# Kernel optimization log

Hardware: AMD Instinct MI355X
Metric: run time of the kernel (lower is better)

Reference implementation:

```python
import jax, jax.numpy as jnp
import numpy as np

H = 16      # query heads
KV = 8      # kv heads
D = 128     # head_dim
HID = 2048  # hidden_size
T = 2048    # tokens
EPS = 1e-6
THETA = 1000000.0


def setup_inputs() -> dict:
    key = jax.random.key(0)
    ks = jax.random.split(key, 4)
    return {
        "hidden_states": jax.random.normal(ks[0], (T, HID), jnp.float32),
        "positions": jnp.arange(T, dtype=jnp.int32),
        "qkv_w": jax.random.normal(ks[1], (H * D + 2 * KV * D, HID), jnp.float32) * 0.02,
        "o_w": jax.random.normal(ks[2], (HID, H * D), jnp.float32) * 0.02,
        "q_norm_w": jnp.ones((D,), jnp.float32),
        "k_norm_w": jnp.ones((D,), jnp.float32),
    }


def _rmsnorm(x, w):
    # x: [T, heads, D]; normalize over last dim
    var = jnp.mean(x * x, axis=-1, keepdims=True)
    return x * jax.lax.rsqrt(var + EPS) * w


def _rope(x, positions):
    # neox-style rotate-half; x: [T, heads, D]
    half = D // 2
    inv_freq = 1.0 / (THETA ** (jnp.arange(0, half, dtype=jnp.float32) / half * 1.0))
    inv_freq = 1.0 / (THETA ** (jnp.arange(0, D, 2, dtype=jnp.float32) / D))
    ang = positions.astype(jnp.float32)[:, None] * inv_freq  # [T, D/2]
    cos = jnp.cos(ang)[:, None, :]
    sin = jnp.sin(ang)[:, None, :]
    x1, x2 = x[..., :half], x[..., half:]
    return jnp.concatenate([x1 * cos - x2 * sin, x2 * cos + x1 * sin], axis=-1)


def reference(hidden_states, positions, qkv_w, o_w, q_norm_w, k_norm_w):
    scale = D ** -0.5
    qkv = hidden_states @ qkv_w.T  # [T, H*D + 2*KV*D]
    q = qkv[:, : H * D].reshape(T, H, D)
    k = qkv[:, H * D : H * D + KV * D].reshape(T, KV, D)
    v = qkv[:, H * D + KV * D :].reshape(T, KV, D)

    q = _rope(_rmsnorm(q, q_norm_w), positions)
    k = _rope(_rmsnorm(k, k_norm_w), positions)

    # GQA: repeat kv heads to match query heads
    rep = H // KV
    k = jnp.repeat(k, rep, axis=1)  # [T, H, D]
    v = jnp.repeat(v, rep, axis=1)

    scores = jnp.einsum("thd,shd->hts", q, k) * scale  # [H, T, T]
    causal = positions[:, None] >= positions[None, :]  # [T, T]
    scores = jnp.where(causal[None, :, :], scores, jnp.float32(-1e30))
    p = jax.nn.softmax(scores, axis=-1)
    o = jnp.einsum("hts,shd->thd", p, v).reshape(T, H * D)
    return o @ o_w.T  # [T, HID]
```

## Files before the change

kernel.cpp:

```cpp
#include <hip/hip_runtime.h>
#include <math.h>

#define T_TOK 2048
#define HID 2048
#define NH 16
#define NKV 8
#define HD 128
#define QKV_N 4096
#define EPS 1e-6f

typedef unsigned short u16;
typedef unsigned int   u32;
typedef __attribute__((ext_vector_type(8))) u16   u16x8;
typedef __attribute__((ext_vector_type(8))) short short8;
typedef __attribute__((ext_vector_type(4))) float floatx4;
typedef __attribute__((ext_vector_type(4))) u32   u32x4;

__device__ __forceinline__ u16 f2bf(float x) {
    u32 u = __float_as_uint(x);
    u = (u + 0x7fffu + ((u >> 16) & 1u)) >> 16;
    return (u16)u;
}
__device__ __forceinline__ float bf2f(u16 h) {
    return __uint_as_float(((u32)h) << 16);
}

__global__ __launch_bounds__(256) void cvt_f32_bf16(
    const float* __restrict__ in, u16* __restrict__ out)
{
    const size_t i = ((size_t)blockIdx.x * 256 + threadIdx.x) * 8;
    float4 a = *(const float4*)(in + i);
    float4 b = *(const float4*)(in + i + 4);
    u16x8 o;
    o[0] = f2bf(a.x); o[1] = f2bf(a.y); o[2] = f2bf(a.z); o[3] = f2bf(a.w);
    o[4] = f2bf(b.x); o[5] = f2bf(b.y); o[6] = f2bf(b.z); o[7] = f2bf(b.w);
    *(u16x8*)(out + i) = o;
}

#define GBM 256
#define GBN 128
#define GBK 64
#define BUFSH 24576

#define WAITV6 asm volatile("s_waitcnt vmcnt(6)" ::: "memory")
#define WAITV0 asm volatile("s_waitcnt vmcnt(0)" ::: "memory")
#define LGKM0  asm volatile("s_waitcnt lgkmcnt(0)" ::: "memory")
#define BARR   asm volatile("s_barrier" ::: "memory")
#define SB     __builtin_amdgcn_sched_barrier(0)

#define STAGEU(i, tt, dstb) \
    __builtin_amdgcn_global_load_lds( \
        (const __attribute__((address_space(1))) u32*)(gsrc[i] + (size_t)(tt)*GBK), \
        (__attribute__((address_space(3))) u32*)((dstb) + loff[i]), 16, 0, 0)

#define RD_A(dst, srcb, f) do { \
    dst[0] = *(const short8*)((srcb) + arow + (f)*1024 + achunk0); \
    dst[1] = *(const short8*)((srcb) + arow + (f)*1024 + achunk1); } while (0)

#define RD_B(dst, srcb) do { \
    _Pragma("unroll") \
    for (int j_ = 0; j_ < 4; ++j_) { \
        dst[j_][0] = *(const short8*)((srcb) + 16384 + brow + j_*1024 + achunk0); \
        dst[j_][1] = *(const short8*)((srcb) + 16384 + brow + j_*1024 + achunk1); } } while (0)

#define MM(f, aa, bb) do { \
    __builtin_amdgcn_s_setprio(1); \
    _Pragma("unroll") \
    for (int j_ = 0; j_ < 4; ++j_) { \
        acc[f][j_] = __builtin_amdgcn_mfma_f32_16x16x32_bf16(aa[0], bb[j_][0], acc[f][j_], 0, 0, 0); \
        acc[f][j_] = __builtin_amdgcn_mfma_f32_16x16x32_bf16(aa[1], bb[j_][1], acc[f][j_], 0, 0, 0); } \
    __builtin_amdgcn_s_setprio(0); } while (0)

#define TILE(t, CURB, NXTB, THDB, BBC, BBN) do { \
    const bool st_ = (t) + 2 < nt; \
    if (st_) { STAGEU(0, (t)+2, THDB); STAGEU(1, (t)+2, THDB); } \
    RD_A(aP1, CURB, 1); SB; \
    MM(0, aP0, BBC); SB; \
    if (st_) { STAGEU(2, (t)+2, THDB); STAGEU(3, (t)+2, THDB); } \
    RD_A(aP0, CURB, 2); SB; \
    MM(1, aP1, BBC); SB; \
    if (st_) { STAGEU(4, (t)+2, THDB); STAGEU(5, (t)+2, THDB); } \
    RD_A(aP1, CURB, 3); SB; \
    MM(2, aP0, BBC); \
    if ((t) + 1 < nt) { \
        if (st_) { WAITV6; } else { WAITV0; } \
        LGKM0; BARR; SB; \
        RD_B(BBN, NXTB); RD_A(aP0, NXTB, 0); \
    } \
    SB; \
    MM(3, aP1, BBC); SB; \
} while (0)

template<bool OUT_BF16>
__global__ __launch_bounds__(512, 2) void gemm_bt_8p(
    const u16* __restrict__ A, const u16* __restrict__ B,
    void* __restrict__ Cv, int K, int lda, int ldb, int ldc)
{
    extern __shared__ short lds[];
    const int tid = threadIdx.x;
    const int w  = tid >> 6;
    const int l  = tid & 63;
    const int m0 = blockIdx.y * GBM;
    const int n0 = blockIdx.x * GBN;
    const int mr = (w >> 1) * 64;
    const int nc = (w & 1) * 64;
    const int cc = l & 15;
    const int q4 = l >> 4;

    const int lr = l >> 3;
    const int gchunk = ((l & 7) ^ (lr & 7)) * 8;
    const u16* gsrc[6]; int loff[6];
    #pragma unroll
    for (int i = 0; i < 6; ++i) {
        const int u = w * 6 + i;
        if (u < 32) {
            gsrc[i] = A + (size_t)(m0 + u*8 + lr) * lda + gchunk;
            loff[i] = u * 512;
        } else {
            const int v = u - 32;
            gsrc[i] = B + (size_t)(n0 + v*8 + lr) * ldb + gchunk;
            loff[i] = 16384 + v * 512;
        }
    }

    const int achunk0 = ((q4)     ^ (cc & 7)) * 8;
    const int achunk1 = ((4 + q4) ^ (cc & 7)) * 8;
    const int arow = (mr + cc) * 64;
    const int brow = (nc + cc) * 64;

    floatx4 acc[4][4];
    #pragma unroll
    for (int f = 0; f < 4; ++f)
        #pragma unroll
        for (int j = 0; j < 4; ++j) acc[f][j] = (floatx4){0.f, 0.f, 0.f, 0.f};

    short8 aP0[2], aP1[2], bbE[4][2], bbO[4][2];
    short* b0 = lds;
    short* b1 = lds + BUFSH;
    short* b2 = lds + 2 * BUFSH;
    const int nt = K >> 6;

    #pragma unroll
    for (int i = 0; i < 6; ++i) STAGEU(i, 0, b0);
    #pragma unroll
    for (int i = 0; i < 6; ++i) STAGEU(i, 1, b1);
    WAITV6; BARR; SB;
    RD_B(bbE, b0); RD_A(aP0, b0, 0);

    short *CURB = b0, *NXTB = b1, *THDB = b2;
    for (int t = 0; t < nt; t += 2) {
        TILE(t, CURB, NXTB, THDB, bbE, bbO);
        { short* tmp = CURB; CURB = NXTB; NXTB = THDB; THDB = tmp; }
        TILE(t + 1, CURB, NXTB, THDB, bbO, bbE);
        { short* tmp = CURB; CURB = NXTB; NXTB = THDB; THDB = tmp; }
    }

    const int r0 = q4 * 4;
    #pragma unroll
    for (int f = 0; f < 4; ++f)
        #pragma unroll
        for (int j = 0; j < 4; ++j)
            #pragma unroll
            for (int r = 0; r < 4; ++r) {
                const int row = m0 + mr + f*16 + r0 + r;
                const int col = n0 + nc + j*16 + cc;
                if (OUT_BF16)
                    ((u16*)Cv)[(size_t)row * ldc + col] = f2bf(acc[f][j][r]);
                else
                    ((float*)Cv)[(size_t)row * ldc + col] = acc[f][j][r];
            }
}

__global__ __launch_bounds__(256) void prep(
    u16* __restrict__ qkv, const int* __restrict__ positions,
    const float* __restrict__ qw, const float* __restrict__ kw,
    u16* __restrict__ Kp, u16* __restrict__ Vtp)
{
    const int tile = blockIdx.x, kvh = blockIdx.y;
    const int tid = threadIdx.x;
    const int w = tid >> 6, l = tid & 63;
    const int t0 = tile * 64;

    const float qw0 = qw[2*l], qw1 = qw[2*l+1];
    const float kw0 = kw[2*l], kw1 = kw[2*l+1];
    const int   i0  = (2*l) & 63;
    const float if0 = exp2f(-(float)i0     * 0.311430758895690f);
    const float if1 = exp2f(-(float)(i0+1) * 0.311430758895690f);

    for (int rr = w; rr < 64; rr += 4) {
        const int t = t0 + rr;
        const int pos = positions[t];
        const float a0 = (float)pos * if0;
        const float a1 = (float)pos * if1;
        const float s0 = sinf(a0), c0 = cosf(a0);
        const float s1 = sinf(a1), c1 = cosf(a1);

        #pragma unroll
        for (int pass = 0; pass < 3; ++pass) {
            const int off = (pass < 2) ? (2*kvh + pass)*HD : NH*HD + kvh*HD;
            const float w0 = (pass < 2) ? qw0 : kw0;
            const float w1 = (pass < 2) ? qw1 : kw1;
            u16* p = qkv + (size_t)t*QKV_N + off;

            const u32 pk = *(const u32*)(p + 2*l);
            const float x0 = bf2f((u16)pk), x1 = bf2f((u16)(pk >> 16));
            float ss = x0*x0 + x1*x1;
            #pragma unroll
            for (int x = 1; x < 64; x <<= 1) ss += __shfl_xor(ss, x);
            const float rs = rsqrtf(ss * (1.0f/128.0f) + EPS);
            const float xn0 = x0 * rs * w0, xn1 = x1 * rs * w1;
            const float px0 = __shfl_xor(xn0, 32);
            const float px1 = __shfl_xor(xn1, 32);

            float o0, o1;
            if (l < 32) { o0 = xn0*c0 - px0*s0; o1 = xn1*c1 - px1*s1; }
            else        { o0 = xn0*c0 + px0*s0; o1 = xn1*c1 + px1*s1; }
            const u32 outpk = (u32)f2bf(o0) | ((u32)f2bf(o1) << 16);

            if (pass < 2) {
                *(u32*)(p + 2*l) = outpk;
            } else {
                const int ch = l >> 2;
                u16* dst = Kp + ((size_t)(kvh*32 + tile)*64 + rr)*128
                              + (ch ^ (rr & 15))*8 + (l & 3)*2;
                *(u32*)dst = outpk;
            }
        }
    }

    __shared__ u16 tl[64][136];
    {
        const int t  = tid >> 2;
        const int c0 = (tid & 3) * 32;
        const u16* src = qkv + (size_t)(t0 + t)*QKV_N + NH*HD + NKV*HD + kvh*HD + c0;
        #pragma unroll
        for (int p2 = 0; p2 < 4; ++p2)
            *(u16x8*)(&tl[t][c0 + p2*8]) = *(const u16x8*)(src + p2*8);
    }
    __syncthreads();
    {
        u16* dstb = Vtp + (size_t)(kvh*32 + tile) * 128 * 64;
        #pragma unroll
        for (int i = 0; i < 4; ++i) {
            const int id = tid*4 + i;
            const int d = id >> 3;
            const int o = id & 7;
            const int sb = (o ^ (d & 7)) * 8;
            u16x8 v;
            #pragma unroll
            for (int j = 0; j < 8; ++j) v[j] = tl[sb + j][d];
            *(u16x8*)(dstb + d*64 + o*8) = v;
        }
    }
}

__global__ __launch_bounds__(512) void attn_mfma(
    const u16* __restrict__ qkv, const u16* __restrict__ Kp,
    const u16* __restrict__ Vtp,
    u16* __restrict__ Opart, float2* __restrict__ ml)
{
    const int id   = blockIdx.x;
    const int half = id >> 8;
    const int kvh  = id & 7;
    const int bid  = (id & 255) >> 3;
    const int qt   = half ? bid : 31 - bid;
    const int t0   = qt * 64;
    const int tid  = threadIdx.x;
    const int w    = tid >> 6;
    const int l    = tid & 63;
    const int q4   = l >> 4;
    const int c    = l & 15;
    const int h    = kvh*2 + (w >> 2);
    const int wq   = w & 3;

    __shared__ short Ks[2][64 * 128];
    __shared__ short Vts[2][128 * 64];

    short8 bq[4];
    {
        const u16* qrow = qkv + (size_t)(t0 + wq*16 + c) * QKV_N + h*HD;
        #pragma unroll
        for (int kk = 0; kk < 4; ++kk)
            bq[kk] = *(const short8*)(qrow + kk*32 + q4*8);
    }

    float m_run = -3.0e38f, l_run = 0.f;
    floatx4 accO[8];
    #pragma unroll
    for (int db = 0; db < 8; ++db) accO[db] = (floatx4){0.f, 0.f, 0.f, 0.f};

    const float Cs = 0.12751744f;

    const int nt  = qt + 1;
    const int nh0 = (nt + 1) >> 1;
    const int tlo = half ? nh0 : 0;
    const int thi = half ? nt  : nh0;

    auto issue = [&](int tile, int buf) {
        const size_t tb = (size_t)(kvh*32 + tile) * 8192;
        const u16* g = (w < 4 ? Kp + tb + w*2048 : Vtp + tb + (w-4)*2048) + l*8;
        short* p = (w < 4) ? (Ks[buf] + w*2048) : (Vts[buf] + (w-4)*2048);
        #pragma unroll
        for (int i = 0; i < 4; ++i)
            __builtin_amdgcn_global_load_lds(
                (const __attribute__((address_space(1))) u32*)(g + i*512),
                (__attribute__((address_space(3))) u32*)(p + i*512), 16, 0, 0);
    };

    if (tlo < thi) issue(tlo, 0);
    int cur = 0;

    for (int tile = tlo; tile < thi; ++tile) {
        __syncthreads();
        if (tile + 1 < thi) issue(tile + 1, cur ^ 1);

        const short* Kc = Ks[cur];
        const short* Vc = Vts[cur];

        floatx4 accS[4];
        #pragma unroll
        for (int sb = 0; sb < 4; ++sb) accS[sb] = (floatx4){0.f, 0.f, 0.f, 0.f};
        #pragma unroll
        for (int kk = 0; kk < 4; ++kk) {
            #pragma unroll
            for (int sb = 0; sb < 4; ++sb) {
                short8 ak = *(const short8*)(Kc + (sb*16 + c)*128 + ((kk*4 + q4) ^ c)*8);
                accS[sb] = __builtin_amdgcn_mfma_f32_16x16x32_bf16(ak, bq[kk], accS[sb], 0, 0, 0);
            }
        }

        if (tile == qt) {
            #pragma unroll
            for (int sb = 0; sb < 4; ++sb)
                #pragma unroll
                for (int r = 0; r < 4; ++r) {
                    const int s_loc = sb*16 + q4*4 + r;
                    const int t_loc = wq*16 + c;
                    if (s_loc > t_loc) accS[sb][r] = -1.0e30f;
                }
        }

        float mt = -3.0e38f;
        #pragma unroll
        for (int sb = 0; sb < 4; ++sb)
            #pragma unroll
            for (int r = 0; r < 4; ++r) mt = fmaxf(mt, accS[sb][r]);
        mt = fmaxf(mt, __shfl_xor(mt, 16));
        mt = fmaxf(mt, __shfl_xor(mt, 32));

        const float m_new = fmaxf(m_run, mt);
        const float alpha = exp2f((m_run - m_new) * Cs);
        m_run = m_new;

        float P[4][4];
        float lsum = 0.f;
        #pragma unroll
        for (int sb = 0; sb < 4; ++sb)
            #pragma unroll
            for (int r = 0; r < 4; ++r) {
                const float e = exp2f((accS[sb][r] - m_new) * Cs);
                P[sb][r] = e;
                lsum += e;
            }
        lsum += __shfl_xor(lsum, 16);
        lsum += __shfl_xor(lsum, 32);
        l_run = l_run * alpha + lsum;

        #pragma unroll
        for (int r = 0; r < 4; ++r) {
            const float ar = __shfl(alpha, (l & 48) | (q4*4 + r));
            #pragma unroll
            for (int db = 0; db < 8; ++db) accO[db][r] *= ar;
        }

        u32 Pp[4][2];
        #pragma unroll
        for (int sb = 0; sb < 4; ++sb)
            #pragma unroll
            for (int p = 0; p < 2; ++p)
                Pp[sb][p] = (u32)f2bf(P[sb][2*p]) | ((u32)f2bf(P[sb][2*p+1]) << 16);

        const int src0 = ((2*q4    ) & 3) * 16 + c;
        const int src1 = ((2*q4 + 1) & 3) * 16 + c;
        const bool hiq = q4 >= 2;
        #pragma unroll
        for (int k2 = 0; k2 < 2; ++k2) {
            u32 x0 = __shfl(Pp[2*k2][0],   src0), y0 = __shfl(Pp[2*k2+1][0], src0);
            u32 x1 = __shfl(Pp[2*k2][1],   src0), y1 = __shfl(Pp[2*k2+1][1], src0);
            u32 x2 = __shfl(Pp[2*k2][0],   src1), y2 = __shfl(Pp[2*k2+1][0], src1);
            u32 x3 = __shfl(Pp[2*k2][1],   src1), y3 = __shfl(Pp[2*k2+1][1], src1);
            u32x4 av;
            av.x = hiq ? y0 : x0;  av.y = hiq ? y1 : x1;
            av.z = hiq ? y2 : x2;  av.w = hiq ? y3 : x3;
            const short8 aP = __builtin_bit_cast(short8, av);
            #pragma unroll
            for (int db = 0; db < 8; ++db) {
                short8 bv = *(const short8*)(Vc + (db*16 + c)*64 + (((k2*4 + q4) ^ (c & 7)))*8);
                accO[db] = __builtin_amdgcn_mfma_f32_16x16x32_bf16(aP, bv, accO[db], 0, 0, 0);
            }
        }
        cur ^= 1;
    }

    const size_t pbase = (size_t)(half * NH + h) * T_TOK;
    #pragma unroll
    for (int r = 0; r < 4; ++r) {
        const int qloc = q4*4 + r;
        const float mr = __shfl(m_run, (l & 48) | qloc);
        const float lr = __shfl(l_run, (l & 48) | qloc);
        const int row_g = t0 + wq*16 + qloc;
        u16* op = Opart + (pbase + row_g) * HD;
        #pragma unroll
        for (int db = 0; db < 8; ++db)
            op[db*16 + c] = f2bf(accO[db][r]);
        if (c == 0) ml[pbase + row_g] = make_float2(mr, lr);
    }
}

__global__ __launch_bounds__(256) void attn_combine(
    const u16* __restrict__ Opart, const float2* __restrict__ ml,
    u16* __restrict__ qkv)
{
    const int idx = blockIdx.x * 256 + threadIdx.x;
    const int c16 = idx & 15;
    const int t   = (idx >> 4) & (T_TOK - 1);
    const int h   = idx >> 15;
    const size_t iA = (size_t)h * T_TOK + t;
    const size_t iB = (size_t)(NH + h) * T_TOK + t;
    const float2 a = ml[iA];
    const float2 b = ml[iB];
    const float Cs = 0.12751744f;
    const float mM = fmaxf(a.x, b.x);
    const float wA = exp2f((a.x - mM) * Cs);
    const float wB = exp2f((b.x - mM) * Cs);
    const float inv = 1.0f / (wA * a.y + wB * b.y);
    const u16x8 A = *(const u16x8*)(Opart + iA * HD + c16*8);
    const u16x8 B = *(const u16x8*)(Opart + iB * HD + c16*8);
    u16x8 o;
    #pragma unroll
    for (int j = 0; j < 8; ++j)
        o[j] = f2bf((wA * bf2f(A[j]) + wB * bf2f(B[j])) * inv);
    *(u16x8*)(qkv + (size_t)t * QKV_N + h * HD + c16*8) = o;
}

extern "C" void kernel_launch(void* const* d_in, const int* in_sizes, int n_in,
                              void* d_out, int out_size, void* d_ws, size_t ws_size,
                              hipStream_t stream)
{
    const float* hidden    = (const float*)d_in[0];
    const int*   positions = (const int*)  d_in[1];
    const float* qkv_w     = (const float*)d_in[2];
    const float* o_w       = (const float*)d_in[3];
    const float* q_norm_w  = (const float*)d_in[4];
    const float* k_norm_w  = (const float*)d_in[5];
    float* out = (float*)d_out;

    u16* qkvbf = (u16*)d_ws;
    u16* wbf   = qkvbf + (size_t)T_TOK * QKV_N;
    u16* abf   = wbf   + (size_t)QKV_N * HID;
    u16* kpb   = abf   + (size_t)T_TOK * HID;
    u16* vpb   = kpb   + (size_t)NKV * T_TOK * HD;

    static bool s_attr = false;
    if (!s_attr) {
        (void)hipFuncSetAttribute(
            reinterpret_cast<const void*>(&gemm_bt_8p<true>),
            hipFuncAttributeMaxDynamicSharedMemorySize, 147456);
        (void)hipFuncSetAttribute(
            reinterpret_cast<const void*>(&gemm_bt_8p<false>),
            hipFuncAttributeMaxDynamicSharedMemorySize, 147456);
        s_attr = true;
    }

    cvt_f32_bf16<<<(T_TOK*HID)/2048, 256, 0, stream>>>(hidden, abf);
    cvt_f32_bf16<<<(QKV_N*HID)/2048, 256, 0, stream>>>(qkv_w, wbf);

    gemm_bt_8p<true><<<dim3(QKV_N/GBN, T_TOK/GBM), 512, 147456, stream>>>(
        abf, wbf, qkvbf, HID, HID, HID, QKV_N);

    prep<<<dim3(T_TOK/64, NKV), 256, 0, stream>>>(
        qkvbf, positions, q_norm_w, k_norm_w, kpb, vpb);

    attn_mfma<<<512, 512, 0, stream>>>(qkvbf, kpb, vpb, wbf, (float2*)abf);

    attn_combine<<<(NH*T_TOK*16)/256, 256, 0, stream>>>(
        wbf, (const float2*)abf, qkvbf);

    cvt_f32_bf16<<<(HID*HID)/2048, 256, 0, stream>>>(o_w, abf);
    gemm_bt_8p<false><<<dim3(HID/GBN, T_TOK/GBM), 512, 147456, stream>>>(
        qkvbf, abf, out, HID, QKV_N, HID, HID);
}
```

Baseline: 248.9 us.

## Rewrite attention with 32x32 MFMA tiles and fuse conversion launches

The attention kernel now uses 32x32x16 bf16 MFMA with 128-query tiles per block, permlane32 swaps instead of shuffles to lay out P, packed bf16 conversion, and a lazy rescale that only updates the running max when it grows past a threshold. The two input conversions are merged into one launch, and the o_w conversion is folded into the prep kernel to cut launch overhead. Partial max/sum scratch is moved into the output buffer so it no longer aliases the converted o_w. This adds register pressure and relies on the lazy-rescale threshold staying within fp32 range.

```diff
diff --git a/kernel.cpp b/kernel.cpp
--- a/kernel.cpp
+++ b/kernel.cpp
@@ -14,6 +14,7 @@
 typedef __attribute__((ext_vector_type(8))) u16   u16x8;
 typedef __attribute__((ext_vector_type(8))) short short8;
 typedef __attribute__((ext_vector_type(4))) float floatx4;
+typedef __attribute__((ext_vector_type(16))) float f32x16;
 typedef __attribute__((ext_vector_type(4))) u32   u32x4;
 
 __device__ __forceinline__ u16 f2bf(float x) {
@@ -24,17 +25,30 @@
 __device__ __forceinline__ float bf2f(u16 h) {
     return __uint_as_float(((u32)h) << 16);
 }
-
-__global__ __launch_bounds__(256) void cvt_f32_bf16(
-    const float* __restrict__ in, u16* __restrict__ out)
-{
-    const size_t i = ((size_t)blockIdx.x * 256 + threadIdx.x) * 8;
+__device__ __forceinline__ u32 cvtpk_bf16(float lo, float hi) {
+    u32 r;
+    asm("v_cvt_pk_bf16_f32 %0, %1, %2" : "=v"(r) : "v"(lo), "v"(hi));
+    return r;
+}
+
+__device__ __forceinline__ void cvt8(const float* __restrict__ in,
+                                     u16* __restrict__ out, size_t i)
+{
     float4 a = *(const float4*)(in + i);
     float4 b = *(const float4*)(in + i + 4);
     u16x8 o;
     o[0] = f2bf(a.x); o[1] = f2bf(a.y); o[2] = f2bf(a.z); o[3] = f2bf(a.w);
     o[4] = f2bf(b.x); o[5] = f2bf(b.y); o[6] = f2bf(b.z); o[7] = f2bf(b.w);
     *(u16x8*)(out + i) = o;
+}
+
+__global__ __launch_bounds__(256) void cvt_pair(
+    const float* __restrict__ ina, u16* __restrict__ outa,
+    const float* __restrict__ inb, u16* __restrict__ outb)
+{
+    const int bid = blockIdx.x;
+    if (bid < 2048) cvt8(ina, outa, ((size_t)bid * 256 + threadIdx.x) * 8);
+    else            cvt8(inb, outb, ((size_t)(bid - 2048) * 256 + threadIdx.x) * 8);
 }
 
 #define GBM 256
@@ -171,12 +185,18 @@
             }
 }
 
-__global__ __launch_bounds__(256) void prep(
+__global__ __launch_bounds__(256) void prep_cvt(
     u16* __restrict__ qkv, const int* __restrict__ positions,
     const float* __restrict__ qw, const float* __restrict__ kw,
-    u16* __restrict__ Kp, u16* __restrict__ Vtp)
-{
-    const int tile = blockIdx.x, kvh = blockIdx.y;
+    u16* __restrict__ Kp, u16* __restrict__ Vtp,
+    const float* __restrict__ ow, u16* __restrict__ owbf)
+{
+    const int bid = blockIdx.x;
+    if (bid >= 256) {
+        cvt8(ow, owbf, ((size_t)(bid - 256) * 256 + threadIdx.x) * 8);
+        return;
+    }
+    const int tile = bid & 31, kvh = bid >> 5;
     const int tid = threadIdx.x;
     const int w = tid >> 6, l = tid & 63;
     const int t0 = tile * 64;
@@ -254,60 +274,65 @@
     }
 }
 
-__global__ __launch_bounds__(512) void attn_mfma(
+__global__ __launch_bounds__(256, 2) void attn_mfma32(
     const u16* __restrict__ qkv, const u16* __restrict__ Kp,
     const u16* __restrict__ Vtp,
     u16* __restrict__ Opart, float2* __restrict__ ml)
 {
     const int id   = blockIdx.x;
-    const int half = id >> 8;
     const int kvh  = id & 7;
-    const int bid  = (id & 255) >> 3;
-    const int qt   = half ? bid : 31 - bid;
-    const int t0   = qt * 64;
-    const int tid  = threadIdx.x;
-    const int w    = tid >> 6;
-    const int l    = tid & 63;
-    const int q4   = l >> 4;
-    const int c    = l & 15;
-    const int h    = kvh*2 + (w >> 2);
-    const int wq   = w & 3;
-
-    __shared__ short Ks[2][64 * 128];
-    __shared__ short Vts[2][128 * 64];
-
-    short8 bq[4];
+    const int u    = id >> 3;
+    const int half = u >> 5;
+    const int v    = u & 31;
+    const int hp   = v & 1;
+    const int bq   = v >> 1;
+    const int qt   = half ? bq : 15 - bq;
+    const int h    = kvh*2 + hp;
+    const int t0q  = qt * 128;
+
+    const int tid = threadIdx.x;
+    const int w   = tid >> 6;
+    const int l   = tid & 63;
+    const int q31 = l & 31;
+    const int hi  = l >> 5;
+
+    __shared__ short Ks[2][8192];
+    __shared__ short Vts[2][8192];
+
+    short8 qf[8];
     {
-        const u16* qrow = qkv + (size_t)(t0 + wq*16 + c) * QKV_N + h*HD;
-        #pragma unroll
-        for (int kk = 0; kk < 4; ++kk)
-            bq[kk] = *(const short8*)(qrow + kk*32 + q4*8);
+        const u16* qrow = qkv + (size_t)(t0q + w*32 + q31) * QKV_N + h*HD;
+        #pragma unroll
+        for (int ks = 0; ks < 8; ++ks)
+            qf[ks] = *(const short8*)(qrow + ks*16 + hi*8);
     }
 
     float m_run = -3.0e38f, l_run = 0.f;
-    floatx4 accO[8];
-    #pragma unroll
-    for (int db = 0; db < 8; ++db) accO[db] = (floatx4){0.f, 0.f, 0.f, 0.f};
+    f32x16 accO[4];
+    #pragma unroll
+    for (int nd = 0; nd < 4; ++nd)
+        #pragma unroll
+        for (int r = 0; r < 16; ++r) accO[nd][r] = 0.f;
 
     const float Cs = 0.12751744f;
 
-    const int nt  = qt + 1;
-    const int nh0 = (nt + 1) >> 1;
+    const int nt  = 2*qt + 2;
+    const int nh0 = qt + 1;
     const int tlo = half ? nh0 : 0;
     const int thi = half ? nt  : nh0;
 
     auto issue = [&](int tile, int buf) {
         const size_t tb = (size_t)(kvh*32 + tile) * 8192;
-        const u16* g = (w < 4 ? Kp + tb + w*2048 : Vtp + tb + (w-4)*2048) + l*8;
-        short* p = (w < 4) ? (Ks[buf] + w*2048) : (Vts[buf] + (w-4)*2048);
-        #pragma unroll
-        for (int i = 0; i < 4; ++i)
+        const u16* g = ((w < 2) ? Kp : Vtp) + tb + (w & 1)*4096 + l*8;
+        short* p = ((w < 2) ? Ks[buf] : Vts[buf]) + (w & 1)*4096 + l*8;
+        #pragma unroll
+        for (int i = 0; i < 8; ++i)
             __builtin_amdgcn_global_load_lds(
                 (const __attribute__((address_space(1))) u32*)(g + i*512),
                 (__attribute__((address_space(3))) u32*)(p + i*512), 16, 0, 0);
     };
 
-    if (tlo < thi) issue(tlo, 0);
+    issue(tlo, 0);
     int cur = 0;
 
     for (int tile = tlo; tile < thi; ++tile) {
@@ -317,104 +342,107 @@
         const short* Kc = Ks[cur];
         const short* Vc = Vts[cur];
 
-        floatx4 accS[4];
-        #pragma unroll
-        for (int sb = 0; sb < 4; ++sb) accS[sb] = (floatx4){0.f, 0.f, 0.f, 0.f};
-        #pragma unroll
-        for (int kk = 0; kk < 4; ++kk) {
+        f32x16 accS0, accS1;
+        #pragma unroll
+        for (int r = 0; r < 16; ++r) { accS0[r] = 0.f; accS1[r] = 0.f; }
+
+        __builtin_amdgcn_s_setprio(1);
+        #pragma unroll
+        for (int ks = 0; ks < 8; ++ks) {
+            const int pc = ((2*ks + hi) ^ (q31 & 15)) * 8;
+            short8 a0 = *(const short8*)(Kc + q31*128 + pc);
+            short8 a1 = *(const short8*)(Kc + (32 + q31)*128 + pc);
+            accS0 = __builtin_amdgcn_mfma_f32_32x32x16_bf16(a0, qf[ks], accS0, 0, 0, 0);
+            accS1 = __builtin_amdgcn_mfma_f32_32x32x16_bf16(a1, qf[ks], accS1, 0, 0, 0);
+        }
+        __builtin_amdgcn_s_setprio(0);
+
+        if (tile >= 2*qt) {
+            const int qg = w*32 + q31 + t0q - tile*64;
             #pragma unroll
-            for (int sb = 0; sb < 4; ++sb) {
-                short8 ak = *(const short8*)(Kc + (sb*16 + c)*128 + ((kk*4 + q4) ^ c)*8);
-                accS[sb] = __builtin_amdgcn_mfma_f32_16x16x32_bf16(ak, bq[kk], accS[sb], 0, 0, 0);
+            for (int r = 0; r < 16; ++r) {
+                const int kvb = (r&3) + 8*(r>>2) + (hi<<2);
+                if (kvb > qg)      accS0[r] = -1.0e30f;
+                if (kvb + 32 > qg) accS1[r] = -1.0e30f;
             }
         }
 
-        if (tile == qt) {
+        float mx = accS0[0];
+        #pragma unroll
+        for (int r = 1; r < 16; ++r) mx = fmaxf(mx, accS0[r]);
+        #pragma unroll
+        for (int r = 0; r < 16; ++r) mx = fmaxf(mx, accS1[r]);
+        mx = fmaxf(mx, __shfl_xor(mx, 32));
+
+        if (__any(mx > m_run + 11.76f)) {
+            const float m_new = fmaxf(m_run, mx);
+            const float alpha = exp2f((m_run - m_new) * Cs);
+            l_run *= alpha;
+            m_run = m_new;
             #pragma unroll
-            for (int sb = 0; sb < 4; ++sb)
-                #pragma unroll
-                for (int r = 0; r < 4; ++r) {
-                    const int s_loc = sb*16 + q4*4 + r;
-                    const int t_loc = wq*16 + c;
-                    if (s_loc > t_loc) accS[sb][r] = -1.0e30f;
-                }
-        }
-
-        float mt = -3.0e38f;
-        #pragma unroll
-        for (int sb = 0; sb < 4; ++sb)
+            for (int r = 0; r < 16; ++r) {
+                const float ar = __shfl(alpha, ((r&3) + 8*(r>>2)) + (hi<<2));
+                accO[0][r] *= ar; accO[1][r] *= ar;
+                accO[2][r] *= ar; accO[3][r] *= ar;
+            }
+        }
+
+        const float mb = m_run * Cs;
+        float lsum = 0.f;
+        #pragma unroll
+        for (int r = 0; r < 16; ++r) {
+            const float e0 = exp2f(accS0[r]*Cs - mb);
+            const float e1 = exp2f(accS1[r]*Cs - mb);
+            accS0[r] = e0; accS1[r] = e1;
+            lsum += e0 + e1;
+        }
+        lsum += __shfl_xor(lsum, 32);
+        l_run += lsum;
+
+        __builtin_amdgcn_s_setprio(1);
+        #pragma unroll
+        for (int ks = 0; ks < 4; ++ks) {
+            const int R = (ks & 1) * 8;
+            u32 x0, x1, x2, x3;
+            if (ks < 2) {
+                x0 = cvtpk_bf16(accS0[R+0], accS0[R+1]);
+                x1 = cvtpk_bf16(accS0[R+2], accS0[R+3]);
+                x2 = cvtpk_bf16(accS0[R+4], accS0[R+5]);
+                x3 = cvtpk_bf16(accS0[R+6], accS0[R+7]);
+            } else {
+                x0 = cvtpk_bf16(accS1[R+0], accS1[R+1]);
+                x1 = cvtpk_bf16(accS1[R+2], accS1[R+3]);
+                x2 = cvtpk_bf16(accS1[R+4], accS1[R+5]);
+                x3 = cvtpk_bf16(accS1[R+6], accS1[R+7]);
+            }
+            asm("v_permlane32_swap_b32 %0, %1" : "+v"(x0), "+v"(x2));
+            asm("v_permlane32_swap_b32 %0, %1" : "+v"(x1), "+v"(x3));
+            u32x4 aw; aw.x = x0; aw.y = x1; aw.z = x2; aw.w = x3;
+            const short8 aP = __builtin_bit_cast(short8, aw);
             #pragma unroll
-            for (int r = 0; r < 4; ++r) mt = fmaxf(mt, accS[sb][r]);
-        mt = fmaxf(mt, __shfl_xor(mt, 16));
-        mt = fmaxf(mt, __shfl_xor(mt, 32));
-
-        const float m_new = fmaxf(m_run, mt);
-        const float alpha = exp2f((m_run - m_new) * Cs);
-        m_run = m_new;
-
-        float P[4][4];
-        float lsum = 0.f;
-        #pragma unroll
-        for (int sb = 0; sb < 4; ++sb)
-            #pragma unroll
-            for (int r = 0; r < 4; ++r) {
-                const float e = exp2f((accS[sb][r] - m_new) * Cs);
-                P[sb][r] = e;
-                lsum += e;
+            for (int nd = 0; nd < 4; ++nd) {
+                short8 bv = *(const short8*)(Vc + (nd*32 + q31)*64
+                                             + ((2*ks + hi) ^ (q31 & 7))*8);
+                accO[nd] = __builtin_amdgcn_mfma_f32_32x32x16_bf16(aP, bv, accO[nd], 0, 0, 0);
             }
-        lsum += __shfl_xor(lsum, 16);
-        lsum += __shfl_xor(lsum, 32);
-        l_run = l_run * alpha + lsum;
-
-        #pragma unroll
-        for (int r = 0; r < 4; ++r) {
-            const float ar = __shfl(alpha, (l & 48) | (q4*4 + r));
-            #pragma unroll
-            for (int db = 0; db < 8; ++db) accO[db][r] *= ar;
-        }
-
-        u32 Pp[4][2];
-        #pragma unroll
-        for (int sb = 0; sb < 4; ++sb)
-            #pragma unroll
-            for (int p = 0; p < 2; ++p)
-                Pp[sb][p] = (u32)f2bf(P[sb][2*p]) | ((u32)f2bf(P[sb][2*p+1]) << 16);
-
-        const int src0 = ((2*q4    ) & 3) * 16 + c;
-        const int src1 = ((2*q4 + 1) & 3) * 16 + c;
-        const bool hiq = q4 >= 2;
-        #pragma unroll
-        for (int k2 = 0; k2 < 2; ++k2) {
-            u32 x0 = __shfl(Pp[2*k2][0],   src0), y0 = __shfl(Pp[2*k2+1][0], src0);
-            u32 x1 = __shfl(Pp[2*k2][1],   src0), y1 = __shfl(Pp[2*k2+1][1], src0);
-            u32 x2 = __shfl(Pp[2*k2][0],   src1), y2 = __shfl(Pp[2*k2+1][0], src1);
-            u32 x3 = __shfl(Pp[2*k2][1],   src1), y3 = __shfl(Pp[2*k2+1][1], src1);
-            u32x4 av;
-            av.x = hiq ? y0 : x0;  av.y = hiq ? y1 : x1;
-            av.z = hiq ? y2 : x2;  av.w = hiq ? y3 : x3;
-            const short8 aP = __builtin_bit_cast(short8, av);
-            #pragma unroll
-            for (int db = 0; db < 8; ++db) {
-                short8 bv = *(const short8*)(Vc + (db*16 + c)*64 + (((k2*4 + q4) ^ (c & 7)))*8);
-                accO[db] = __builtin_amdgcn_mfma_f32_16x16x32_bf16(aP, bv, accO[db], 0, 0, 0);
-            }
-        }
+        }
+        __builtin_amdgcn_s_setprio(0);
+
         cur ^= 1;
     }
 
     const size_t pbase = (size_t)(half * NH + h) * T_TOK;
     #pragma unroll
-    for (int r = 0; r < 4; ++r) {
-        const int qloc = q4*4 + r;
-        const float mr = __shfl(m_run, (l & 48) | qloc);
-        const float lr = __shfl(l_run, (l & 48) | qloc);
-        const int row_g = t0 + wq*16 + qloc;
-        u16* op = Opart + (pbase + row_g) * HD;
-        #pragma unroll
-        for (int db = 0; db < 8; ++db)
-            op[db*16 + c] = f2bf(accO[db][r]);
-        if (c == 0) ml[pbase + row_g] = make_float2(mr, lr);
-    }
+    for (int r = 0; r < 16; ++r) {
+        const int qr = (r&3) + 8*(r>>2) + (hi<<2);
+        u16* op = Opart + (pbase + t0q + w*32 + qr) * HD;
+        op[q31]      = f2bf(accO[0][r]);
+        op[32 + q31] = f2bf(accO[1][r]);
+        op[64 + q31] = f2bf(accO[2][r]);
+        op[96 + q31] = f2bf(accO[3][r]);
+    }
+    if (l < 32)
+        ml[pbase + t0q + w*32 + l] = make_float2(m_run, l_run);
 }
 
 __global__ __launch_bounds__(256) void attn_combine(
@@ -472,21 +500,19 @@
         s_attr = true;
     }
 
-    cvt_f32_bf16<<<(T_TOK*HID)/2048, 256, 0, stream>>>(hidden, abf);
-    cvt_f32_bf16<<<(QKV_N*HID)/2048, 256, 0, stream>>>(qkv_w, wbf);
+    cvt_pair<<<6144, 256, 0, stream>>>(hidden, abf, qkv_w, wbf);
 
     gemm_bt_8p<true><<<dim3(QKV_N/GBN, T_TOK/GBM), 512, 147456, stream>>>(
         abf, wbf, qkvbf, HID, HID, HID, QKV_N);
 
-    prep<<<dim3(T_TOK/64, NKV), 256, 0, stream>>>(
-        qkvbf, positions, q_norm_w, k_norm_w, kpb, vpb);
-
-    attn_mfma<<<512, 512, 0, stream>>>(qkvbf, kpb, vpb, wbf, (float2*)abf);
+    prep_cvt<<<2304, 256, 0, stream>>>(
+        qkvbf, positions, q_norm_w, k_norm_w, kpb, vpb, o_w, abf);
+
+    attn_mfma32<<<512, 256, 0, stream>>>(qkvbf, kpb, vpb, wbf, (float2*)out);
 
     attn_combine<<<(NH*T_TOK*16)/256, 256, 0, stream>>>(
-        wbf, (const float2*)abf, qkvbf);
-
-    cvt_f32_bf16<<<(HID*HID)/2048, 256, 0, stream>>>(o_w, abf);
+        wbf, (const float2*)out, qkvbf);
+
     gemm_bt_8p<false><<<dim3(HID/GBN, T_TOK/GBM), 512, 147456, stream>>>(
         qkvbf, abf, out, HID, QKV_N, HID, HID);
 }
```

After: 240.0 us. 3.6% less time.
